# Performance work log

Hardware: AMD Instinct MI355X
Metric: run time of the kernel (lower is better)

## Reference

```python
import jax, jax.numpy as jnp
import numpy as np

N_NODES = 100000
N_EDGES = 1600000
IN_F = 256
OUT_F = 128


def setup_inputs() -> dict:
    key = jax.random.key(0)
    k_x, k_w, k_r, k_c, k_v = jax.random.split(key, 5)
    x = jax.random.normal(k_x, (N_NODES, IN_F), dtype=jnp.float32)
    weight = jax.random.normal(k_w, (IN_F, OUT_F), dtype=jnp.float32) * (1.0 / np.sqrt(IN_F))
    edge_row = jax.random.randint(k_r, (N_EDGES,), 0, N_NODES, dtype=jnp.int32)
    edge_col = jax.random.randint(k_c, (N_EDGES,), 0, N_NODES, dtype=jnp.int32)
    edge_vals = jax.random.uniform(k_v, (N_EDGES,), dtype=jnp.float32)
    return {"x": x, "weight": weight, "edge_row": edge_row,
            "edge_col": edge_col, "edge_vals": edge_vals}


def reference(x, weight, edge_row, edge_col, edge_vals):
    # Dense projection: h = x @ W  (torch: self.linear(x), bias=False)
    h = x @ weight                                   # [N, OUT_F]
    # SpMM: out[i] = sum_{(i,j) in E} A_hat[i,j] * h[j]
    messages = edge_vals[:, None] * h[edge_col]      # [E, OUT_F] gather
    out = jax.ops.segment_sum(messages, edge_row, num_segments=N_NODES)
    return out
```

## Files before the change

### kernel.cpp

```cpp
#include <hip/hip_runtime.h>
#include <hip/hip_bf16.h>


#define IN_F  256
#define OUT_F 128
#define BSH   6
#define CH    4096
#define CAP   1536

typedef __attribute__((ext_vector_type(8))) short sh8;
typedef __attribute__((ext_vector_type(4))) float f32x4;

__device__ __forceinline__ unsigned short f2bf(float f) {
    unsigned u = __float_as_uint(f);
    unsigned r = u + 0x7fff + ((u >> 16) & 1);
    return (unsigned short)(r >> 16);
}
__device__ __forceinline__ float bf2f(unsigned short s) {
    return __uint_as_float(((unsigned)s) << 16);
}

__global__ __launch_bounds__(256) void wt_prep_kernel(
    const float* __restrict__ w, unsigned short* __restrict__ wt) {
    int i = blockIdx.x * 256 + threadIdx.x;
    int k = i >> 7, n = i & 127;
    wt[n * IN_F + k] = f2bf(w[i]);
}

__global__ __launch_bounds__(256) void gemm_mfma_kernel(
    const float* __restrict__ x, const unsigned short* __restrict__ wt,
    unsigned short* __restrict__ h, int n_nodes) {
    int tid = threadIdx.x;
    int wv = tid >> 6, l = tid & 63;
    int l16 = l & 15, lk = (l >> 4) * 8;
    long row0 = (long)blockIdx.x * 128 + wv * 32;

    long rmax = n_nodes - 1;
    long ra0 = row0 + l16;      if (ra0 > rmax) ra0 = rmax;
    long ra1 = row0 + 16 + l16; if (ra1 > rmax) ra1 = rmax;
    const float* xp0 = x + ra0 * IN_F + lk;
    const float* xp1 = x + ra1 * IN_F + lk;
    const unsigned short* wp = wt + l16 * IN_F + lk;

    f32x4 acc[2][8];
    #pragma unroll
    for (int rt = 0; rt < 2; rt++)
        #pragma unroll
        for (int nt = 0; nt < 8; nt++)
            acc[rt][nt] = (f32x4){0.f, 0.f, 0.f, 0.f};

    #pragma unroll
    for (int ks = 0; ks < 8; ks++) {
        int k0 = ks * 32;
        float4 t0 = *(const float4*)(xp0 + k0);
        float4 t1 = *(const float4*)(xp0 + k0 + 4);
        float4 t2 = *(const float4*)(xp1 + k0);
        float4 t3 = *(const float4*)(xp1 + k0 + 4);
        sh8 a0, a1;
        a0[0] = (short)f2bf(t0.x); a0[1] = (short)f2bf(t0.y);
        a0[2] = (short)f2bf(t0.z); a0[3] = (short)f2bf(t0.w);
        a0[4] = (short)f2bf(t1.x); a0[5] = (short)f2bf(t1.y);
        a0[6] = (short)f2bf(t1.z); a0[7] = (short)f2bf(t1.w);
        a1[0] = (short)f2bf(t2.x); a1[1] = (short)f2bf(t2.y);
        a1[2] = (short)f2bf(t2.z); a1[3] = (short)f2bf(t2.w);
        a1[4] = (short)f2bf(t3.x); a1[5] = (short)f2bf(t3.y);
        a1[6] = (short)f2bf(t3.z); a1[7] = (short)f2bf(t3.w);
        #pragma unroll
        for (int nt = 0; nt < 8; nt++) {
            sh8 b = *(const sh8*)(wp + nt * 16 * IN_F + k0);
            acc[0][nt] = __builtin_amdgcn_mfma_f32_16x16x32_bf16(
                a0, b, acc[0][nt], 0, 0, 0);
            acc[1][nt] = __builtin_amdgcn_mfma_f32_16x16x32_bf16(
                a1, b, acc[1][nt], 0, 0, 0);
        }
    }

    int rbase = (l >> 4) * 4;
    #pragma unroll
    for (int rt = 0; rt < 2; rt++) {
        #pragma unroll
        for (int j = 0; j < 4; j++) {
            long r = row0 + rt * 16 + rbase + j;
            if (r < n_nodes) {
                unsigned short* hp = h + r * OUT_F + l16;
                #pragma unroll
                for (int nt = 0; nt < 8; nt++)
                    hp[nt * 16] = f2bf(acc[rt][nt][j]);
            }
        }
    }
}

__global__ __launch_bounds__(256) void hist_kernel(
    const int* __restrict__ erow, int* __restrict__ T,
    int n_edges, int nbuck) {
    __shared__ int lh[2048];
    int tid = threadIdx.x, b = blockIdx.x;
    for (int k = tid; k < nbuck; k += 256) lh[k] = 0;
    __syncthreads();
    int s = b * CH, e = min(s + CH, n_edges);
    for (int i = s + tid; i < e; i += 256)
        atomicAdd(&lh[erow[i] >> BSH], 1);
    __syncthreads();
    int* Tr = T + (long)b * nbuck;
    for (int k = tid; k < nbuck; k += 256) Tr[k] = lh[k];
}

__global__ __launch_bounds__(256) void colscan_kernel(
    int* __restrict__ T, int* __restrict__ colTotal, int nblk, int nbuck) {
    int k = blockIdx.x * 4 + (threadIdx.x >> 6);
    int lane = threadIdx.x & 63;
    if (k >= nbuck) return;
    int carry = 0;
    for (int c = 0; c < nblk; c += 64) {
        int b = c + lane;
        int v = (b < nblk) ? T[(long)b * nbuck + k] : 0;
        int incl = v;
        #pragma unroll
        for (int off = 1; off < 64; off <<= 1) {
            int t = __shfl_up(incl, off);
            if (lane >= off) incl += t;
        }
        if (b < nblk) T[(long)b * nbuck + k] = carry + incl - v;
        carry += __shfl(incl, 63);
    }
    if (lane == 0) colTotal[k] = carry;
}

__global__ __launch_bounds__(256) void basescan_kernel(
    const int* __restrict__ colTotal, int* __restrict__ base, int nbuck) {
    __shared__ int s[256];
    int tid = threadIdx.x;
    int loc[8];
    int sum = 0;
    #pragma unroll
    for (int j = 0; j < 8; j++) {
        int i = tid * 8 + j;
        loc[j] = (i < nbuck) ? colTotal[i] : 0;
        sum += loc[j];
    }
    s[tid] = sum;
    __syncthreads();
    for (int off = 1; off < 256; off <<= 1) {
        int t = (tid >= off) ? s[tid - off] : 0;
        __syncthreads();
        s[tid] += t;
        __syncthreads();
    }
    int pre = s[tid] - sum;
    #pragma unroll
    for (int j = 0; j < 8; j++) {
        int i = tid * 8 + j;
        if (i < nbuck) base[i] = pre;
        pre += loc[j];
    }
    if (tid == 255) base[nbuck] = pre;
}

__global__ __launch_bounds__(256) void scatter_kernel(
    const int* __restrict__ erow, const int* __restrict__ ecol,
    const float* __restrict__ eval, const int* __restrict__ T,
    const int* __restrict__ base, unsigned long long* __restrict__ epack,
    int n_edges, int nbuck) {
    __shared__ int lpos[2048];
    int tid = threadIdx.x, b = blockIdx.x;
    const int* Tr = T + (long)b * nbuck;
    for (int k = tid; k < nbuck; k += 256) lpos[k] = base[k] + Tr[k];
    __syncthreads();
    int s = b * CH, e = min(s + CH, n_edges);
    for (int i = s + tid; i < e; i += 256) {
        int r = erow[i];
        int c = ecol[i];
        float v = eval[i];
        int p = atomicAdd(&lpos[r >> BSH], 1);
        epack[p] = ((unsigned long long)__float_as_uint(v) << 32)
                 | ((unsigned)(r & 63) << 17) | (unsigned)c;
    }
}

__global__ __launch_bounds__(256) void bucket_rowsum_kernel(
    const unsigned short* __restrict__ h, const int* __restrict__ base,
    const unsigned long long* __restrict__ epack,
    float* __restrict__ out, int n_nodes, int nbuck) {
    __shared__ unsigned long long sorted[CAP];
    __shared__ int lh[64], lo[64], lc[64];
    int tid = threadIdx.x, k = blockIdx.x;
    int s = base[k], e = base[k + 1];
    int size = e - s;
    int wv = tid >> 6, lane = tid & 63;

    if (tid < 64) { lh[tid] = 0; lc[tid] = 0; }
    __syncthreads();
    for (int i = tid; i < size; i += 256) {
        unsigned lo32 = (unsigned)(epack[s + i] & 0xffffffffu);
        atomicAdd(&lh[(lo32 >> 17) & 63], 1);
    }
    __syncthreads();
    if (tid < 64) {
        int v = lh[tid];
        int incl = v;
        #pragma unroll
        for (int off = 1; off < 64; off <<= 1) {
            int t = __shfl_up(incl, off);
            if (lane >= off) incl += t;
        }
        lo[tid] = incl - v;
    }
    __syncthreads();
    bool fits = (size <= CAP);
    if (fits) {
        for (int i = tid; i < size; i += 256) {
            unsigned long long ed = epack[s + i];
            int r = (int)((ed >> 17) & 63);
            int p = atomicAdd(&lc[r], 1) + lo[r];
            sorted[p] = ed;
        }
    }
    __syncthreads();

    for (int rr = 0; rr < 16; rr++) {
        int r = wv * 16 + rr;
        long row = (long)k * 64 + r;
        if (row >= n_nodes) break;
        int rs = lo[r], cnt = lh[r];
        float a0 = 0.f, a1 = 0.f;
        if (fits) {
            int j = 0;
            for (; j + 4 <= cnt; j += 4) {
                unsigned long long e0 = sorted[rs + j];
                unsigned long long e1 = sorted[rs + j + 1];
                unsigned long long e2 = sorted[rs + j + 2];
                unsigned long long e3 = sorted[rs + j + 3];
                unsigned hv0 = *((const unsigned*)(h + (long)(e0 & 0x1ffffu) * OUT_F) + lane);
                unsigned hv1 = *((const unsigned*)(h + (long)(e1 & 0x1ffffu) * OUT_F) + lane);
                unsigned hv2 = *((const unsigned*)(h + (long)(e2 & 0x1ffffu) * OUT_F) + lane);
                unsigned hv3 = *((const unsigned*)(h + (long)(e3 & 0x1ffffu) * OUT_F) + lane);
                float v0 = __uint_as_float((unsigned)(e0 >> 32));
                float v1 = __uint_as_float((unsigned)(e1 >> 32));
                float v2 = __uint_as_float((unsigned)(e2 >> 32));
                float v3 = __uint_as_float((unsigned)(e3 >> 32));
                a0 += v0 * bf2f((unsigned short)(hv0 & 0xffff));
                a1 += v0 * bf2f((unsigned short)(hv0 >> 16));
                a0 += v1 * bf2f((unsigned short)(hv1 & 0xffff));
                a1 += v1 * bf2f((unsigned short)(hv1 >> 16));
                a0 += v2 * bf2f((unsigned short)(hv2 & 0xffff));
                a1 += v2 * bf2f((unsigned short)(hv2 >> 16));
                a0 += v3 * bf2f((unsigned short)(hv3 & 0xffff));
                a1 += v3 * bf2f((unsigned short)(hv3 >> 16));
            }
            for (; j < cnt; j++) {
                unsigned long long e0 = sorted[rs + j];
                unsigned hv0 = *((const unsigned*)(h + (long)(e0 & 0x1ffffu) * OUT_F) + lane);
                float v0 = __uint_as_float((unsigned)(e0 >> 32));
                a0 += v0 * bf2f((unsigned short)(hv0 & 0xffff));
                a1 += v0 * bf2f((unsigned short)(hv0 >> 16));
            }
        } else {
            for (int i = 0; i < size; i++) {
                unsigned long long ed = epack[s + i];
                if ((int)((ed >> 17) & 63) == r) {
                    unsigned hv0 = *((const unsigned*)(h + (long)(ed & 0x1ffffu) * OUT_F) + lane);
                    float v0 = __uint_as_float((unsigned)(ed >> 32));
                    a0 += v0 * bf2f((unsigned short)(hv0 & 0xffff));
                    a1 += v0 * bf2f((unsigned short)(hv0 >> 16));
                }
            }
        }
        float2 o; o.x = a0; o.y = a1;
        *(float2*)(out + row * OUT_F + lane * 2) = o;
    }
}

extern "C" void kernel_launch(void* const* d_in, const int* in_sizes, int n_in,
                              void* d_out, int out_size, void* d_ws, size_t ws_size,
                              hipStream_t stream) {
    const float* x    = (const float*)d_in[0];
    const float* w    = (const float*)d_in[1];
    const int*   erow = (const int*)d_in[2];
    const int*   ecol = (const int*)d_in[3];
    const float* eval = (const float*)d_in[4];
    float* out = (float*)d_out;

    int n_nodes = in_sizes[0] / IN_F;
    int n_edges = in_sizes[2];
    int nbuck = (n_nodes + 63) >> BSH;
    int nblk  = (n_edges + CH - 1) / CH;

    char* p = (char*)d_ws;
    auto alloc = [&](size_t bytes) {
        char* q = p;
        p += (bytes + 255) & ~(size_t)255;
        return q;
    };
    unsigned short* h  = (unsigned short*)alloc((size_t)n_nodes * OUT_F * 2);
    int* T        = (int*)alloc((size_t)nblk * nbuck * 4);
    int* colTotal = (int*)alloc((size_t)nbuck * 4);
    int* base     = (int*)alloc((size_t)(nbuck + 1) * 4);
    unsigned long long* epack = (unsigned long long*)alloc((size_t)n_edges * 8);
    unsigned short* wt = (unsigned short*)alloc((size_t)IN_F * OUT_F * 2);

    wt_prep_kernel<<<dim3((IN_F * OUT_F) / 256), 256, 0, stream>>>(w, wt);
    gemm_mfma_kernel<<<dim3((n_nodes + 127) / 128), 256, 0, stream>>>(
        x, wt, h, n_nodes);

    hist_kernel<<<dim3(nblk), 256, 0, stream>>>(erow, T, n_edges, nbuck);
    colscan_kernel<<<dim3((nbuck + 3) / 4), 256, 0, stream>>>(
        T, colTotal, nblk, nbuck);
    basescan_kernel<<<dim3(1), 256, 0, stream>>>(colTotal, base, nbuck);
    scatter_kernel<<<dim3(nblk), 256, 0, stream>>>(
        erow, ecol, eval, T, base, epack, n_edges, nbuck);

    bucket_rowsum_kernel<<<dim3(nbuck), 256, 0, stream>>>(
        h, base, epack, out, n_nodes, nbuck);
}
```

Baseline: 166.2 us.

## Stage x tiles into LDS via async global_load_lds with XOR swizzle in GEMM

```diff
diff --git a/kernel.cpp b/kernel.cpp
--- a/kernel.cpp
+++ b/kernel.cpp
@@ -30,63 +30,65 @@
 __global__ __launch_bounds__(256) void gemm_mfma_kernel(
     const float* __restrict__ x, const unsigned short* __restrict__ wt,
     unsigned short* __restrict__ h, int n_nodes) {
+    __shared__ float xs[64 * 256];
     int tid = threadIdx.x;
-    int wv = tid >> 6, l = tid & 63;
-    int l16 = l & 15, lk = (l >> 4) * 8;
-    long row0 = (long)blockIdx.x * 128 + wv * 32;
-
+    int w = tid >> 6, lane = tid & 63;
+    long blk0 = (long)blockIdx.x * 64;
     long rmax = n_nodes - 1;
-    long ra0 = row0 + l16;      if (ra0 > rmax) ra0 = rmax;
-    long ra1 = row0 + 16 + l16; if (ra1 > rmax) ra1 = rmax;
-    const float* xp0 = x + ra0 * IN_F + lk;
-    const float* xp1 = x + ra1 * IN_F + lk;
-    const unsigned short* wp = wt + l16 * IN_F + lk;
-
-    f32x4 acc[2][8];
-    #pragma unroll
-    for (int rt = 0; rt < 2; rt++)
-        #pragma unroll
-        for (int nt = 0; nt < 8; nt++)
-            acc[rt][nt] = (f32x4){0.f, 0.f, 0.f, 0.f};
+
+    #pragma unroll
+    for (int r = 0; r < 16; r++) {
+        int row = r * 4 + w;
+        int lg = lane ^ (row & 15);
+        long grow = blk0 + row; if (grow > rmax) grow = rmax;
+        const float* src = x + grow * IN_F + lg * 4;
+        __builtin_amdgcn_global_load_lds(
+            (const __attribute__((address_space(1))) void*)src,
+            (__attribute__((address_space(3))) void*)((char*)xs + row * 1024),
+            16, 0, 0);
+    }
+    __syncthreads();
+
+    int l16 = lane & 15, hi = lane >> 4;
+    int row_l = w * 16 + l16;
+    const char* xrow = (const char*)xs + row_l * 1024;
+    const unsigned short* wp = wt + l16 * IN_F + hi * 8;
+
+    f32x4 acc[8];
+    #pragma unroll
+    for (int nt = 0; nt < 8; nt++)
+        acc[nt] = (f32x4){0.f, 0.f, 0.f, 0.f};
 
     #pragma unroll
     for (int ks = 0; ks < 8; ks++) {
+        int g0 = hi * 2 + ks * 8;
+        int p0 = g0 ^ l16;
+        int p1 = (g0 + 1) ^ l16;
+        float4 t0 = *(const float4*)(xrow + p0 * 16);
+        float4 t1 = *(const float4*)(xrow + p1 * 16);
+        sh8 a;
+        a[0] = (short)f2bf(t0.x); a[1] = (short)f2bf(t0.y);
+        a[2] = (short)f2bf(t0.z); a[3] = (short)f2bf(t0.w);
+        a[4] = (short)f2bf(t1.x); a[5] = (short)f2bf(t1.y);
+        a[6] = (short)f2bf(t1.z); a[7] = (short)f2bf(t1.w);
         int k0 = ks * 32;
-        float4 t0 = *(const float4*)(xp0 + k0);
-        float4 t1 = *(const float4*)(xp0 + k0 + 4);
-        float4 t2 = *(const float4*)(xp1 + k0);
-        float4 t3 = *(const float4*)(xp1 + k0 + 4);
-        sh8 a0, a1;
-        a0[0] = (short)f2bf(t0.x); a0[1] = (short)f2bf(t0.y);
-        a0[2] = (short)f2bf(t0.z); a0[3] = (short)f2bf(t0.w);
-        a0[4] = (short)f2bf(t1.x); a0[5] = (short)f2bf(t1.y);
-        a0[6] = (short)f2bf(t1.z); a0[7] = (short)f2bf(t1.w);
-        a1[0] = (short)f2bf(t2.x); a1[1] = (short)f2bf(t2.y);
-        a1[2] = (short)f2bf(t2.z); a1[3] = (short)f2bf(t2.w);
-        a1[4] = (short)f2bf(t3.x); a1[5] = (short)f2bf(t3.y);
-        a1[6] = (short)f2bf(t3.z); a1[7] = (short)f2bf(t3.w);
         #pragma unroll
         for (int nt = 0; nt < 8; nt++) {
             sh8 b = *(const sh8*)(wp + nt * 16 * IN_F + k0);
-            acc[0][nt] = __builtin_amdgcn_mfma_f32_16x16x32_bf16(
-                a0, b, acc[0][nt], 0, 0, 0);
-            acc[1][nt] = __builtin_amdgcn_mfma_f32_16x16x32_bf16(
-                a1, b, acc[1][nt], 0, 0, 0);
-        }
-    }
-
-    int rbase = (l >> 4) * 4;
-    #pragma unroll
-    for (int rt = 0; rt < 2; rt++) {
-        #pragma unroll
-        for (int j = 0; j < 4; j++) {
-            long r = row0 + rt * 16 + rbase + j;
-            if (r < n_nodes) {
-                unsigned short* hp = h + r * OUT_F + l16;
-                #pragma unroll
-                for (int nt = 0; nt < 8; nt++)
-                    hp[nt * 16] = f2bf(acc[rt][nt][j]);
-            }
+            acc[nt] = __builtin_amdgcn_mfma_f32_16x16x32_bf16(
+                a, b, acc[nt], 0, 0, 0);
+        }
+    }
+
+    int rbase = hi * 4;
+    #pragma unroll
+    for (int j = 0; j < 4; j++) {
+        long r = blk0 + w * 16 + rbase + j;
+        if (r < n_nodes) {
+            unsigned short* hp = h + r * OUT_F + l16;
+            #pragma unroll
+            for (int nt = 0; nt < 8; nt++)
+                hp[nt * 16] = f2bf(acc[nt][j]);
         }
     }
 }
@@ -300,7 +302,7 @@
     unsigned short* wt = (unsigned short*)alloc((size_t)IN_F * OUT_F * 2);
 
     wt_prep_kernel<<<dim3((IN_F * OUT_F) / 256), 256, 0, stream>>>(w, wt);
-    gemm_mfma_kernel<<<dim3((n_nodes + 127) / 128), 256, 0, stream>>>(
+    gemm_mfma_kernel<<<dim3((n_nodes + 63) / 64), 256, 0, stream>>>(
         x, wt, h, n_nodes);
 
     hist_kernel<<<dim3(nblk), 256, 0, stream>>>(erow, T, n_edges, nbuck);
```

New measurement: 183.0 us. 1.1x slower.
